# Optimization experiments

Hardware: AMD Instinct MI355X
Metric: run time of the kernel (lower is better)

## Reference

```python
import jax, jax.numpy as jnp
import numpy as np

PROCESSING_STEPS = 3


def setup_inputs() -> dict:
    key = jax.random.key(0)
    ks = jax.random.split(key, 6)
    N, D, G = 500000, 128, 4096
    x = jax.random.normal(ks[0], (N, D), dtype=jnp.float32)
    # torch LSTM param layout: [4*hidden, input] and [4*hidden, hidden], gates i,f,g,o
    s = 1.0 / np.sqrt(D)
    W_ih = jax.random.uniform(ks[1], (4 * D, 2 * D), minval=-s, maxval=s, dtype=jnp.float32)
    W_hh = jax.random.uniform(ks[2], (4 * D, D), minval=-s, maxval=s, dtype=jnp.float32)
    b_ih = jax.random.uniform(ks[3], (4 * D,), minval=-s, maxval=s, dtype=jnp.float32)
    b_hh = jax.random.uniform(ks[4], (4 * D,), minval=-s, maxval=s, dtype=jnp.float32)
    index = jnp.sort(jax.random.randint(ks[5], (N,), 0, G, dtype=jnp.int64))
    return {"x": x, "W_ih": W_ih, "W_hh": W_hh, "b_ih": b_ih, "b_hh": b_hh,
            "index": index, "dim_size": G}


def _lstm_cell(inp, h, c, W_ih, W_hh, b_ih, b_hh):
    gates = inp @ W_ih.T + h @ W_hh.T + (b_ih + b_hh)  # [G, 4D]
    i, f, g, o = jnp.split(gates, 4, axis=-1)
    c = jax.nn.sigmoid(f) * c + jax.nn.sigmoid(i) * jnp.tanh(g)
    h = jax.nn.sigmoid(o) * jnp.tanh(c)
    return h, c


def reference(x, W_ih, W_hh, b_ih, b_hh, index, dim_size):
    N, D = x.shape
    h = jnp.zeros((dim_size, D), dtype=x.dtype)
    c = jnp.zeros((dim_size, D), dtype=x.dtype)
    q_star = jnp.zeros((dim_size, 2 * D), dtype=x.dtype)
    for _ in range(PROCESSING_STEPS):
        h, c = _lstm_cell(q_star, h, c, W_ih, W_hh, b_ih, b_hh)
        q = h  # [G, D]
        e = jnp.sum(x * q[index], axis=-1)  # [N]
        # segment softmax (numerically stable)
        m = jax.ops.segment_max(e, index, num_segments=dim_size)
        m = jnp.where(jnp.isfinite(m), m, 0.0)  # guard empty segments
        ex = jnp.exp(e - m[index])
        s = jax.ops.segment_sum(ex, index, num_segments=dim_size)
        a = ex / jnp.maximum(s, 1e-16)[index]  # [N]
        r = jax.ops.segment_sum(a[:, None] * x, index, num_segments=dim_size)  # [G, D]
        q_star = jnp.concatenate([q, r], axis=-1)
    return q_star
```

## Files before the change

kernel.cpp:

```cpp
#include <hip/hip_runtime.h>
#include <math.h>

#define D 128

__device__ __forceinline__ float sigmoidf_(float x) { return 1.f / (1.f + __expf(-x)); }

__global__ void seg_bounds_kernel(const int* __restrict__ idx, int N, int G,
                                  int* __restrict__ seg_off) {
    int g = blockIdx.x * blockDim.x + threadIdx.x;
    if (g > G) return;
    int lo = 0, hi = N;
    while (lo < hi) {
        int mid = (lo + hi) >> 1;
        if (idx[mid] < g) lo = mid + 1; else hi = mid;
    }
    seg_off[g] = lo;
}

__global__ void prep_wc_kernel(const float* __restrict__ W_ih, const float* __restrict__ W_hh,
                               float* __restrict__ Wc) {
    int t = blockIdx.x * blockDim.x + threadIdx.x;
    if (t >= 4 * D * D) return;
    int j = t >> 7;
    int k = t & (D - 1);
    Wc[t] = W_ih[(size_t)j * (2 * D) + k] + W_hh[t];
}

__global__ void prep_bias_kernel(const float* __restrict__ b_ih, const float* __restrict__ b_hh,
                                 float* __restrict__ b_sum, float* __restrict__ h1,
                                 float* __restrict__ c1) {
    int t = threadIdx.x;
    float b = b_ih[t] + b_hh[t];
    b_sum[t] = b;
    if (t < D) {
        float bi = b_ih[t] + b_hh[t];
        float bg = b_ih[2 * D + t] + b_hh[2 * D + t];
        float bo = b_ih[3 * D + t] + b_hh[3 * D + t];
        float c = sigmoidf_(bi) * tanhf(bg);
        c1[t] = c;
        h1[t] = sigmoidf_(bo) * tanhf(c);
    }
}

__global__ void base2_kernel(const float* __restrict__ Wc, const float* __restrict__ b_sum,
                             const float* __restrict__ h1, float* __restrict__ base2) {
    __shared__ float hs[D];
    int j = blockIdx.x * 256 + threadIdx.x;
    if (threadIdx.x < D) hs[threadIdx.x] = h1[threadIdx.x];
    __syncthreads();
    float acc = 0.f;
    const float4* w4 = (const float4*)(Wc + (size_t)j * D);
#pragma unroll 8
    for (int k4 = 0; k4 < D / 4; ++k4) {
        float4 w = w4[k4];
        const float* hp = &hs[k4 * 4];
        acc += w.x * hp[0] + w.y * hp[1] + w.z * hp[2] + w.w * hp[3];
    }
    base2[j] = b_sum[j] + acc;
}

__global__ __launch_bounds__(256) void attn_kernel(
    const float* __restrict__ x,
    const int* __restrict__ seg_off,
    const float* __restrict__ q,
    int q_stride,
    float* __restrict__ r_out, int r_stride,
    int G) {
    int g = blockIdx.x;
    if (g >= G) return;
    int tid = threadIdx.x;
    int wave = tid >> 6, lane = tid & 63;
    int half = lane >> 5;
    int col4 = lane & 31;

    __shared__ float sm[4], ss[4];
    __shared__ float sacc[4][D];

    int start = seg_off[g], end = seg_off[g + 1];
    int count = end - start;
    int chunk = (count + 3) >> 2;
    int wsr = start + wave * chunk;
    int wer = min(wsr + chunk, end);

    const float4* x4 = (const float4*)x;
    const float4* q4 = (const float4*)(q + (size_t)g * q_stride);
    float4 qv = q4[col4];

    float m = -INFINITY, s = 0.f;
    float4 acc = {0.f, 0.f, 0.f, 0.f};

    if (wsr < wer) {
        int r0 = wsr + half; r0 = r0 < wer ? r0 : wer - 1;
        float4 xv = x4[(size_t)r0 * 32 + col4];
        for (int n = wsr; n < wer; n += 2) {
            int r2 = n + 2 + half; r2 = r2 < wer ? r2 : wer - 1;
            float4 xn = x4[(size_t)r2 * 32 + col4];

            float p = xv.x * qv.x + xv.y * qv.y + xv.z * qv.z + xv.w * qv.w;
            p += __shfl_xor(p, 1);
            p += __shfl_xor(p, 2);
            p += __shfl_xor(p, 4);
            p += __shfl_xor(p, 8);
            p += __shfl_xor(p, 16);
            float po = __shfl_xor(p, 32);
            float p0 = half ? po : p;
            float p1 = half ? p : po;
            if (n + 1 >= wer) p1 = -INFINITY;

            float mn = fmaxf(m, fmaxf(p0, p1));
            float al = __expf(m - mn);
            float w0 = __expf(p0 - mn);
            float w1 = __expf(p1 - mn);
            float wsel = half ? w1 : w0;
            s = s * al + w0 + w1;
            acc.x = acc.x * al + wsel * xv.x;
            acc.y = acc.y * al + wsel * xv.y;
            acc.z = acc.z * al + wsel * xv.z;
            acc.w = acc.w * al + wsel * xv.w;
            m = mn;
            xv = xn;
        }
    }
    acc.x += __shfl_xor(acc.x, 32);
    acc.y += __shfl_xor(acc.y, 32);
    acc.z += __shfl_xor(acc.z, 32);
    acc.w += __shfl_xor(acc.w, 32);

    if (lane == 0) { sm[wave] = m; ss[wave] = s; }
    if (half == 0) *(float4*)&sacc[wave][col4 * 4] = acc;
    __syncthreads();

    if (tid < D) {
        float m0 = sm[0], m1 = sm[1], m2 = sm[2], m3 = sm[3];
        float mstar = fmaxf(fmaxf(m0, m1), fmaxf(m2, m3));
        float r = 0.f;
        if (mstar > -INFINITY) {
            float e0 = __expf(m0 - mstar), e1 = __expf(m1 - mstar);
            float e2 = __expf(m2 - mstar), e3 = __expf(m3 - mstar);
            float stot = ss[0] * e0 + ss[1] * e1 + ss[2] * e2 + ss[3] * e3;
            float at = sacc[0][tid] * e0 + sacc[1][tid] * e1
                     + sacc[2][tid] * e2 + sacc[3][tid] * e3;
            r = at / fmaxf(stot, 1e-16f);
        }
        r_out[(size_t)g * r_stride + tid] = r;
    }
}

__global__ __launch_bounds__(256) void gates_gemm_kernel(
    const float* __restrict__ A1,
    const float* __restrict__ W1,
    const float* __restrict__ A2,
    const float* __restrict__ W2,
    int sW2,
    const float* __restrict__ bias,
    float* __restrict__ gates) {
    __shared__ float As[16][132];
    __shared__ float Ws[16][132];
    int t = threadIdx.x;
    int tx = t & 15, ty = t >> 4;
    int g0 = blockIdx.x * 128, j0 = blockIdx.y * 128;
    int lr = t >> 1;
    int lk = (t & 1) * 8;

    float acc[8][8];
#pragma unroll
    for (int i = 0; i < 8; ++i)
#pragma unroll
        for (int j = 0; j < 8; ++j) acc[i][j] = 0.f;

    for (int phase = 0; phase < 2; ++phase) {
        const float* A = phase ? A2 : A1;
        if (A == nullptr) continue;
        const float* W = phase ? W2 : W1;
        int sW = phase ? sW2 : D;
        for (int kk = 0; kk < D; kk += 16) {
            float4 a0 = *(const float4*)&A[(size_t)(g0 + lr) * D + kk + lk];
            float4 a1 = *(const float4*)&A[(size_t)(g0 + lr) * D + kk + lk + 4];
            float4 w0 = *(const float4*)&W[(size_t)(j0 + lr) * sW + kk + lk];
            float4 w1 = *(const float4*)&W[(size_t)(j0 + lr) * sW + kk + lk + 4];
            __syncthreads();
            As[lk + 0][lr] = a0.x; As[lk + 1][lr] = a0.y; As[lk + 2][lr] = a0.z; As[lk + 3][lr] = a0.w;
            As[lk + 4][lr] = a1.x; As[lk + 5][lr] = a1.y; As[lk + 6][lr] = a1.z; As[lk + 7][lr] = a1.w;
            Ws[lk + 0][lr] = w0.x; Ws[lk + 1][lr] = w0.y; Ws[lk + 2][lr] = w0.z; Ws[lk + 3][lr] = w0.w;
            Ws[lk + 4][lr] = w1.x; Ws[lk + 5][lr] = w1.y; Ws[lk + 6][lr] = w1.z; Ws[lk + 7][lr] = w1.w;
            __syncthreads();
#pragma unroll
            for (int k = 0; k < 16; ++k) {
                float4 a0v = *(const float4*)&As[k][ty * 8];
                float4 a1v = *(const float4*)&As[k][ty * 8 + 4];
                float4 b0v = *(const float4*)&Ws[k][tx * 8];
                float4 b1v = *(const float4*)&Ws[k][tx * 8 + 4];
                float av[8] = {a0v.x, a0v.y, a0v.z, a0v.w, a1v.x, a1v.y, a1v.z, a1v.w};
                float bv[8] = {b0v.x, b0v.y, b0v.z, b0v.w, b1v.x, b1v.y, b1v.z, b1v.w};
#pragma unroll
                for (int i = 0; i < 8; ++i)
#pragma unroll
                    for (int j = 0; j < 8; ++j)
                        acc[i][j] = fmaf(av[i], bv[j], acc[i][j]);
            }
        }
    }
#pragma unroll
    for (int i = 0; i < 8; ++i) {
        size_t row = (size_t)(g0 + ty * 8 + i);
        float4 o0, o1;
        int jb = j0 + tx * 8;
        o0.x = acc[i][0] + bias[jb + 0]; o0.y = acc[i][1] + bias[jb + 1];
        o0.z = acc[i][2] + bias[jb + 2]; o0.w = acc[i][3] + bias[jb + 3];
        o1.x = acc[i][4] + bias[jb + 4]; o1.y = acc[i][5] + bias[jb + 5];
        o1.z = acc[i][6] + bias[jb + 6]; o1.w = acc[i][7] + bias[jb + 7];
        *(float4*)&gates[row * 512 + jb] = o0;
        *(float4*)&gates[row * 512 + jb + 4] = o1;
    }
}

__global__ void cell_kernel(const float* __restrict__ gates,
                            const float* __restrict__ c_prev, int c_stride,
                            float* __restrict__ c_out,
                            float* __restrict__ h_out, int h_stride,
                            int total) {
    int t = blockIdx.x * blockDim.x + threadIdx.x;
    if (t >= total) return;
    int g = t >> 7, k = t & (D - 1);
    const float* grow = gates + (size_t)g * 512;
    float ig = grow[k];
    float fg = grow[D + k];
    float gg = grow[2 * D + k];
    float og = grow[3 * D + k];
    float cp = c_prev[(size_t)g * c_stride + k];
    float c = sigmoidf_(fg) * cp + sigmoidf_(ig) * tanhf(gg);
    float h = sigmoidf_(og) * tanhf(c);
    c_out[t] = c;
    h_out[(size_t)g * h_stride + k] = h;
}

extern "C" void kernel_launch(void* const* d_in, const int* in_sizes, int n_in,
                              void* d_out, int out_size, void* d_ws, size_t ws_size,
                              hipStream_t stream) {
    const float* x      = (const float*)d_in[0];
    const float* W_ih   = (const float*)d_in[1];
    const float* W_hh   = (const float*)d_in[2];
    const float* b_ih   = (const float*)d_in[3];
    const float* b_hh   = (const float*)d_in[4];
    const int*   index  = (const int*)d_in[5];
    int N = in_sizes[5];
    int G = out_size / (2 * D);
    float* out = (float*)d_out;

    float* ws = (float*)d_ws;
    float* Wc     = ws;
    float* b_sum  = Wc + 4 * D * D;
    float* h1     = b_sum + 4 * D;
    float* c1     = h1 + D;
    float* base2  = c1 + D;
    float* r1     = base2 + 4 * D;
    float* h2     = r1 + (size_t)G * D;
    float* c2     = h2 + (size_t)G * D;
    float* r2     = c2 + (size_t)G * D;
    float* gatesb = r2 + (size_t)G * D;
    int* seg_off  = (int*)(gatesb + (size_t)G * 4 * D);
    float* c3     = r1;

    seg_bounds_kernel<<<(G + 1 + 255) / 256, 256, 0, stream>>>(index, N, G, seg_off);
    prep_wc_kernel<<<(4 * D * D + 255) / 256, 256, 0, stream>>>(W_ih, W_hh, Wc);
    prep_bias_kernel<<<1, 512, 0, stream>>>(b_ih, b_hh, b_sum, h1, c1);
    base2_kernel<<<2, 256, 0, stream>>>(Wc, b_sum, h1, base2);

    attn_kernel<<<G, 256, 0, stream>>>(x, seg_off, h1, 0, r1, D, G);

    gates_gemm_kernel<<<dim3(G / 128, 4), 256, 0, stream>>>(
        nullptr, Wc, r1, W_ih + D, 2 * D, base2, gatesb);
    cell_kernel<<<(G * D + 255) / 256, 256, 0, stream>>>(gatesb, c1, 0, c2, h2, D, G * D);
    attn_kernel<<<G, 256, 0, stream>>>(x, seg_off, h2, D, r2, D, G);

    gates_gemm_kernel<<<dim3(G / 128, 4), 256, 0, stream>>>(
        h2, Wc, r2, W_ih + D, 2 * D, b_sum, gatesb);
    cell_kernel<<<(G * D + 255) / 256, 256, 0, stream>>>(gatesb, c2, D, c3, out, 2 * D, G * D);
    attn_kernel<<<G, 256, 0, stream>>>(x, seg_off, out, 2 * D, out + D, 2 * D, G);
}
```

Measured before the change: 529.6 us.

## Split fused online-softmax attention into score and weighted-sum kernels

Replaces the single-pass online-softmax attention kernel with two kernels. The first computes and stores the per-row scores; the second computes the segment max and sum from the stored scores and then accumulates the weighted rows of x. Both kernels prefetch four rows deep instead of one. This removes the per-row rescaling exps and the serial max dependency, but each step now reads x twice (256 MB per pass) and adds extra launches and an N-sized score buffer.

Result: slower. 763.9 us (+44.2%).

```diff
diff --git a/kernel.cpp b/kernel.cpp
--- a/kernel.cpp
+++ b/kernel.cpp
@@ -59,101 +59,134 @@
     base2[j] = b_sum[j] + acc;
 }
 
-__global__ __launch_bounds__(256) void attn_kernel(
-    const float* __restrict__ x,
-    const int* __restrict__ seg_off,
-    const float* __restrict__ q,
-    int q_stride,
-    float* __restrict__ r_out, int r_stride,
-    int G) {
+__global__ __launch_bounds__(256) void score_kernel(
+    const float* __restrict__ x, const int* __restrict__ seg_off,
+    const float* __restrict__ q, int q_stride,
+    float* __restrict__ e, int G) {
     int g = blockIdx.x;
     if (g >= G) return;
     int tid = threadIdx.x;
     int wave = tid >> 6, lane = tid & 63;
-    int half = lane >> 5;
-    int col4 = lane & 31;
-
-    __shared__ float sm[4], ss[4];
-    __shared__ float sacc[4][D];
+    int half = lane >> 5, col4 = lane & 31;
 
     int start = seg_off[g], end = seg_off[g + 1];
     int count = end - start;
     int chunk = (count + 3) >> 2;
     int wsr = start + wave * chunk;
     int wer = min(wsr + chunk, end);
+    if (wsr >= wer) return;
 
     const float4* x4 = (const float4*)x;
     const float4* q4 = (const float4*)(q + (size_t)g * q_stride);
     float4 qv = q4[col4];
 
-    float m = -INFINITY, s = 0.f;
+    int np = (wer - wsr + 1) >> 1;
+    float4 buf[4];
+#pragma unroll
+    for (int j = 0; j < 4; ++j) {
+        int ip = j < np ? j : np - 1;
+        int row = wsr + 2 * ip + half; row = row < wer ? row : wer - 1;
+        buf[j] = x4[(size_t)row * 32 + col4];
+    }
+    for (int i = 0; i < np; ++i) {
+        float4 xv = buf[i & 3];
+        int ip = i + 4; ip = ip < np ? ip : np - 1;
+        int rowp = wsr + 2 * ip + half; rowp = rowp < wer ? rowp : wer - 1;
+        buf[i & 3] = x4[(size_t)rowp * 32 + col4];
+
+        float p = xv.x * qv.x + xv.y * qv.y + xv.z * qv.z + xv.w * qv.w;
+        p += __shfl_xor(p, 1);
+        p += __shfl_xor(p, 2);
+        p += __shfl_xor(p, 4);
+        p += __shfl_xor(p, 8);
+        p += __shfl_xor(p, 16);
+        int rs = wsr + 2 * i + half;
+        if (col4 == 0 && rs < wer) e[rs] = p;
+    }
+}
+
+__global__ __launch_bounds__(256) void wsum_kernel(
+    const float* __restrict__ x, const int* __restrict__ seg_off,
+    const float* __restrict__ e,
+    float* __restrict__ r_out, int r_stride, int G) {
+    int g = blockIdx.x;
+    if (g >= G) return;
+    int tid = threadIdx.x;
+    int wave = tid >> 6, lane = tid & 63;
+    int half = lane >> 5, col4 = lane & 31;
+
+    __shared__ float sred[4];
+    __shared__ float sacc[4][D];
+
+    int start = seg_off[g], end = seg_off[g + 1];
+
+    float lm = -INFINITY;
+    for (int i = start + tid; i < end; i += 256) lm = fmaxf(lm, e[i]);
+#pragma unroll
+    for (int off = 1; off < 64; off <<= 1) lm = fmaxf(lm, __shfl_xor(lm, off));
+    if (lane == 0) sred[wave] = lm;
+    __syncthreads();
+    float m = fmaxf(fmaxf(sred[0], sred[1]), fmaxf(sred[2], sred[3]));
+    __syncthreads();
+    float ls = 0.f;
+    for (int i = start + tid; i < end; i += 256) ls += __expf(e[i] - m);
+#pragma unroll
+    for (int off = 1; off < 64; off <<= 1) ls += __shfl_xor(ls, off);
+    if (lane == 0) sred[wave] = ls;
+    __syncthreads();
+    float s = sred[0] + sred[1] + sred[2] + sred[3];
+    float inv = 1.f / fmaxf(s, 1e-16f);
+
+    int count = end - start;
+    int chunk = (count + 3) >> 2;
+    int wsr = start + wave * chunk;
+    int wer = min(wsr + chunk, end);
+
+    const float4* x4 = (const float4*)x;
     float4 acc = {0.f, 0.f, 0.f, 0.f};
 
     if (wsr < wer) {
-        int r0 = wsr + half; r0 = r0 < wer ? r0 : wer - 1;
-        float4 xv = x4[(size_t)r0 * 32 + col4];
-        for (int n = wsr; n < wer; n += 2) {
-            int r2 = n + 2 + half; r2 = r2 < wer ? r2 : wer - 1;
-            float4 xn = x4[(size_t)r2 * 32 + col4];
-
-            float p = xv.x * qv.x + xv.y * qv.y + xv.z * qv.z + xv.w * qv.w;
-            p += __shfl_xor(p, 1);
-            p += __shfl_xor(p, 2);
-            p += __shfl_xor(p, 4);
-            p += __shfl_xor(p, 8);
-            p += __shfl_xor(p, 16);
-            float po = __shfl_xor(p, 32);
-            float p0 = half ? po : p;
-            float p1 = half ? p : po;
-            if (n + 1 >= wer) p1 = -INFINITY;
-
-            float mn = fmaxf(m, fmaxf(p0, p1));
-            float al = __expf(m - mn);
-            float w0 = __expf(p0 - mn);
-            float w1 = __expf(p1 - mn);
-            float wsel = half ? w1 : w0;
-            s = s * al + w0 + w1;
-            acc.x = acc.x * al + wsel * xv.x;
-            acc.y = acc.y * al + wsel * xv.y;
-            acc.z = acc.z * al + wsel * xv.z;
-            acc.w = acc.w * al + wsel * xv.w;
-            m = mn;
-            xv = xn;
+        int np = (wer - wsr + 1) >> 1;
+        float4 xb[4]; float eb[4];
+#pragma unroll
+        for (int j = 0; j < 4; ++j) {
+            int ip = j < np ? j : np - 1;
+            int row = wsr + 2 * ip + half; row = row < wer ? row : wer - 1;
+            xb[j] = x4[(size_t)row * 32 + col4];
+            eb[j] = e[row];
+        }
+        for (int i = 0; i < np; ++i) {
+            float4 xv = xb[i & 3];
+            float ev = eb[i & 3];
+            int ip = i + 4; ip = ip < np ? ip : np - 1;
+            int rowp = wsr + 2 * ip + half; rowp = rowp < wer ? rowp : wer - 1;
+            xb[i & 3] = x4[(size_t)rowp * 32 + col4];
+            eb[i & 3] = e[rowp];
+
+            int rs = wsr + 2 * i + half;
+            float w = (rs < wer) ? __expf(ev - m) * inv : 0.f;
+            acc.x += w * xv.x;
+            acc.y += w * xv.y;
+            acc.z += w * xv.z;
+            acc.w += w * xv.w;
         }
     }
     acc.x += __shfl_xor(acc.x, 32);
     acc.y += __shfl_xor(acc.y, 32);
     acc.z += __shfl_xor(acc.z, 32);
     acc.w += __shfl_xor(acc.w, 32);
-
-    if (lane == 0) { sm[wave] = m; ss[wave] = s; }
     if (half == 0) *(float4*)&sacc[wave][col4 * 4] = acc;
     __syncthreads();
-
     if (tid < D) {
-        float m0 = sm[0], m1 = sm[1], m2 = sm[2], m3 = sm[3];
-        float mstar = fmaxf(fmaxf(m0, m1), fmaxf(m2, m3));
-        float r = 0.f;
-        if (mstar > -INFINITY) {
-            float e0 = __expf(m0 - mstar), e1 = __expf(m1 - mstar);
-            float e2 = __expf(m2 - mstar), e3 = __expf(m3 - mstar);
-            float stot = ss[0] * e0 + ss[1] * e1 + ss[2] * e2 + ss[3] * e3;
-            float at = sacc[0][tid] * e0 + sacc[1][tid] * e1
-                     + sacc[2][tid] * e2 + sacc[3][tid] * e3;
-            r = at / fmaxf(stot, 1e-16f);
-        }
+        float r = sacc[0][tid] + sacc[1][tid] + sacc[2][tid] + sacc[3][tid];
         r_out[(size_t)g * r_stride + tid] = r;
     }
 }
 
 __global__ __launch_bounds__(256) void gates_gemm_kernel(
-    const float* __restrict__ A1,
-    const float* __restrict__ W1,
-    const float* __restrict__ A2,
-    const float* __restrict__ W2,
-    int sW2,
-    const float* __restrict__ bias,
-    float* __restrict__ gates) {
+    const float* __restrict__ A1, const float* __restrict__ W1,
+    const float* __restrict__ A2, const float* __restrict__ W2, int sW2,
+    const float* __restrict__ bias, float* __restrict__ gates) {
     __shared__ float As[16][132];
     __shared__ float Ws[16][132];
     int t = threadIdx.x;
@@ -258,7 +291,8 @@
     float* c2     = h2 + (size_t)G * D;
     float* r2     = c2 + (size_t)G * D;
     float* gatesb = r2 + (size_t)G * D;
-    int* seg_off  = (int*)(gatesb + (size_t)G * 4 * D);
+    float* e_buf  = gatesb + (size_t)G * 4 * D;
+    int* seg_off  = (int*)(e_buf + (size_t)N);
     float* c3     = r1;
 
     seg_bounds_kernel<<<(G + 1 + 255) / 256, 256, 0, stream>>>(index, N, G, seg_off);
@@ -266,15 +300,18 @@
     prep_bias_kernel<<<1, 512, 0, stream>>>(b_ih, b_hh, b_sum, h1, c1);
     base2_kernel<<<2, 256, 0, stream>>>(Wc, b_sum, h1, base2);
 
-    attn_kernel<<<G, 256, 0, stream>>>(x, seg_off, h1, 0, r1, D, G);
+    score_kernel<<<G, 256, 0, stream>>>(x, seg_off, h1, 0, e_buf, G);
+    wsum_kernel<<<G, 256, 0, stream>>>(x, seg_off, e_buf, r1, D, G);
 
     gates_gemm_kernel<<<dim3(G / 128, 4), 256, 0, stream>>>(
         nullptr, Wc, r1, W_ih + D, 2 * D, base2, gatesb);
     cell_kernel<<<(G * D + 255) / 256, 256, 0, stream>>>(gatesb, c1, 0, c2, h2, D, G * D);
-    attn_kernel<<<G, 256, 0, stream>>>(x, seg_off, h2, D, r2, D, G);
+    score_kernel<<<G, 256, 0, stream>>>(x, seg_off, h2, D, e_buf, G);
+    wsum_kernel<<<G, 256, 0, stream>>>(x, seg_off, e_buf, r2, D, G);
 
     gates_gemm_kernel<<<dim3(G / 128, 4), 256, 0, stream>>>(
         h2, Wc, r2, W_ih + D, 2 * D, b_sum, gatesb);
     cell_kernel<<<(G * D + 255) / 256, 256, 0, stream>>>(gatesb, c2, D, c3, out, 2 * D, G * D);
-    attn_kernel<<<G, 256, 0, stream>>>(x, seg_off, out, 2 * D, out + D, 2 * D, G);
-}
+    score_kernel<<<G, 256, 0, stream>>>(x, seg_off, out, 2 * D, e_buf, G);
+    wsum_kernel<<<G, 256, 0, stream>>>(x, seg_off, e_buf, out + D, 2 * D, G);
+}
```
